# Kernel tuning notes

Measured on AMD Instinct MI355X. Metric: run time of the kernel, lower is better.

The kernel has to match this reference:

```python
import jax, jax.numpy as jnp
import numpy as np

EMBEDDING_LOSS_WEIGHT = 1.0
COMMITMENT_LOSS_WEIGHT = 0.25
ENTROPY_LOSS_WEIGHT = 0.02


def setup_inputs() -> dict:
    key = jax.random.key(0)
    k1, k2 = jax.random.split(key)
    inputs = jax.random.normal(k1, (16, 32, 32, 256), dtype=jnp.float32)
    # RandomUniform() default range in keras is [-0.05, 0.05]
    codebook = jax.random.uniform(k2, (4096, 256), dtype=jnp.float32,
                                  minval=-0.05, maxval=0.05)
    return {"inputs": inputs, "codebook": codebook}


def reference(inputs, codebook):
    sg = jax.lax.stop_gradient
    B, H, W, D = inputs.shape
    K = codebook.shape[0]
    flat = inputs.reshape(-1, D)  # [N, D], N = B*H*W

    x_sq = jnp.sum(flat * flat, axis=-1, keepdims=True)          # [N, 1]
    c_sq = jnp.sum(codebook * codebook, axis=-1)                 # [K]
    cross = flat @ codebook.T                                    # [N, K] GEMM
    distances = x_sq + c_sq - 2.0 * cross                        # [N, K]

    tokens = jnp.argmin(distances, axis=-1)                      # [N] int32
    embeddings = jnp.take(codebook, tokens, axis=0).reshape(B, H, W, D)

    embedding_loss = EMBEDDING_LOSS_WEIGHT * jnp.mean((sg(embeddings) - inputs) ** 2)
    commitment_loss = COMMITMENT_LOSS_WEIGHT * jnp.mean((embeddings - sg(inputs)) ** 2)

    # entropy loss: for codebook entries never selected, penalize their
    # minimum distance to any input vector
    active = jnp.zeros((K,), jnp.int32).at[tokens].add(1)        # scatter counts
    min_dist_per_class = jnp.min(distances, axis=0)              # [K]
    entropy_loss = ENTROPY_LOSS_WEIGHT * jnp.mean(
        jnp.where(active == 0, min_dist_per_class, 0.0))

    loss = embedding_loss + commitment_loss + entropy_loss

    # training=True straight-through estimator
    out = inputs + sg(embeddings - inputs)
    return out, loss
```

## Files before the change

### kernel.cpp

```cpp
#include <hip/hip_runtime.h>
#include <stdint.h>


#define N_ROWS 16384
#define DIM    256
#define KCODES 4096
#define NCHUNK 8
#define KC     (KCODES / NCHUNK)
#define TM     128
#define TN     128
#define BK     32
#define NKT    (KC / TN)
#define NDC    (DIM / BK)
#define NSTEP  (NKT * NDC)
#define NGRAN  (NCHUNK * 2)
#define NRB    (N_ROWS / TM)

typedef float    f32x4 __attribute__((ext_vector_type(4)));
typedef _Float16 f16x8 __attribute__((ext_vector_type(8)));

#define GLOAD_LDS16(g, l) __builtin_amdgcn_global_load_lds(                 \
    (const __attribute__((address_space(1))) void*)(g),                     \
    (__attribute__((address_space(3))) void*)(l), 16, 0, 0)

#define WAITVM_(n) asm volatile("s_waitcnt vmcnt(" #n ")" ::: "memory")
#define WAITVM(n)  WAITVM_(n)
#define MEMPIN()   asm volatile("" ::: "memory")

__device__ __forceinline__ unsigned umin_(unsigned a, unsigned b) { return a < b ? a : b; }
__device__ __forceinline__ unsigned umax_(unsigned a, unsigned b) { return a > b ? a : b; }
__device__ __forceinline__ unsigned long long umin64_(unsigned long long a,
                                                      unsigned long long b) {
    return a < b ? a : b;
}
__device__ __forceinline__ unsigned long long umax64_(unsigned long long a,
                                                      unsigned long long b) {
    return a > b ? a : b;
}

__device__ __forceinline__ unsigned fkey(float f) {
    unsigned b = __float_as_uint(f);
    return (b & 0x80000000u) ? ~b : (b | 0x80000000u);
}
__device__ __forceinline__ float fkey_inv(unsigned k) {
    unsigned b = (k & 0x80000000u) ? (k ^ 0x80000000u) : ~k;
    return __uint_as_float(b);
}
__device__ __forceinline__ unsigned short f2h(float f) {
    union { _Float16 h; unsigned short u; } cv;
    cv.h = (_Float16)f;
    return cv.u;
}

__global__ __launch_bounds__(256) void vq_prep_kernel(
        const float* __restrict__ x, const float* __restrict__ cb,
        unsigned short* __restrict__ xh, unsigned short* __restrict__ ch,
        float* __restrict__ xsq, float* __restrict__ csq,
        unsigned* __restrict__ active, double* __restrict__ accum,
        unsigned* __restrict__ counter) {
    const int b = blockIdx.x, t = threadIdx.x;
    if (b < KCODES / 256) {
        int i = b * 256 + t;
        active[i] = 0u;
        if (i == 0) { accum[0] = 0.0; accum[1] = 0.0; counter[0] = 0u; }
    }
    const size_t NX = (size_t)N_ROWS * DIM;
    size_t e = (size_t)b * 1024 + (size_t)t * 4;
    const float* src; unsigned short* dst; float* sq; size_t off;
    if (e < NX) { src = x;  dst = xh; sq = xsq; off = e; }
    else        { src = cb; dst = ch; sq = csq; off = e - NX; }
    float4 v = *(const float4*)(src + off);
    ushort4 h;
    h.x = f2h(v.x); h.y = f2h(v.y); h.z = f2h(v.z); h.w = f2h(v.w);
    *(ushort4*)(dst + off) = h;
    double s = (double)v.x * v.x + (double)v.y * v.y
             + (double)v.z * v.z + (double)v.w * v.w;
    for (int o = 32; o; o >>= 1) s += __shfl_down(s, o);
    if ((t & 63) == 0) sq[off >> 8] = (float)s;
}

__global__ __launch_bounds__(256, 2) void vq_gemm_kernel(
        const unsigned short* __restrict__ xh_g, const unsigned short* __restrict__ ch_g,
        const float* __restrict__ xsq, const float* __restrict__ csq,
        unsigned* __restrict__ colmin_part, uint2* __restrict__ top2_out) {
    __shared__ __align__(16) unsigned short b_lds[4][TN][BK];
    __shared__ float    xsq_l[128];
    __shared__ float    csq_l[KC];
    __shared__ unsigned colmin_l[KC];
    __shared__ uint2    u12_l[16][256];

    const int t = threadIdx.x;
    const int wave = t >> 6, lane = t & 63, quad = lane >> 4, L = lane & 15;
    const int whalf = wave >> 1, chalf = wave & 1;
    const int row0  = blockIdx.x * TM;
    const int code0 = blockIdx.y * KC;

    if (t < 128) xsq_l[t] = xsq[row0 + t];
    csq_l[t]       = csq[code0 + t];
    csq_l[t + 256] = csq[code0 + t + 256];
    colmin_l[t] = 0xFFFFFFFFu; colmin_l[t + 256] = 0xFFFFFFFFu;
#pragma unroll
    for (int i = 0; i < 16; ++i)
        u12_l[i][t] = make_uint2(0xFFFFFFFFu, 0xFFFFFFFFu);

    const unsigned short* abase =
        xh_g + ((size_t)(row0 + whalf * 64 + L) * DIM + quad * 8);

    auto stageB = [&](int buf, int kt_, int dc_) {
        const unsigned short* bsrc =
            ch_g + (size_t)(code0 + kt_ * TN) * DIM + dc_ * BK;
        unsigned short* dst = &b_lds[buf][0][0];
#pragma unroll
        for (int k = 0; k < 2; ++k) {
            const int j = t + k * 256;
            const int r = j >> 2, sg = (j & 3) ^ ((j >> 3) & 3);
            GLOAD_LDS16(bsrc + (size_t)r * DIM + sg * 8, dst + (size_t)j * 8);
        }
    };

    const int bslot = (L >> 1) & 3;

    f16x8 afr[NDC][4];
#pragma unroll
    for (int dc = 0; dc < NDC; ++dc)
#pragma unroll
        for (int mt = 0; mt < 4; ++mt)
            afr[dc][mt] = *(const f16x8*)(abase + (size_t)mt * 16 * DIM + dc * BK);
    MEMPIN();
    stageB(0, 0, 0);
    MEMPIN();
    stageB(1, 0, 1);
    MEMPIN();
    stageB(2, 0, 2);
    MEMPIN();

    asm volatile("s_waitcnt lgkmcnt(0)" ::: "memory");
    __builtin_amdgcn_s_barrier();
    __builtin_amdgcn_sched_barrier(0);

    auto epilogue = [&](int kt, f32x4 (&acc)[4][4]) {
        float csq4[4]; unsigned colf[4];
        float dmin[4] = {3.4e38f, 3.4e38f, 3.4e38f, 3.4e38f};
#pragma unroll
        for (int nt = 0; nt < 4; ++nt) {
            csq4[nt] = csq_l[kt * TN + chalf * 64 + nt * 16 + L];
            colf[nt] = (unsigned)(kt * 128 + chalf * 64 + nt * 16 + L);
        }
#pragma unroll
        for (int mt = 0; mt < 4; ++mt) {
            const f32x4 xq = *(const f32x4*)&xsq_l[whalf * 64 + mt * 16 + quad * 4];
#pragma unroll
            for (int reg = 0; reg < 4; ++reg) {
                const int i = mt * 4 + reg;
                uint2 e = u12_l[i][t];
#pragma unroll
                for (int nt = 0; nt < 4; ++nt) {
                    float s = fmaf(-2.0f, acc[mt][nt][reg], csq4[nt]);
                    unsigned key = (fkey(s) & 0xFFFFFE00u) | colf[nt];
                    unsigned lo = umin_(e.x, key);
                    e.y = umin_(e.y, umax_(e.x, key));
                    e.x = lo;
                    dmin[nt] = fminf(dmin[nt], xq[reg] + s);
                }
                u12_l[i][t] = e;
            }
        }
#pragma unroll
        for (int nt = 0; nt < 4; ++nt) {
            unsigned dk = fkey(dmin[nt]);
            dk = umin_(dk, (unsigned)__shfl_xor((int)dk, 16));
            dk = umin_(dk, (unsigned)__shfl_xor((int)dk, 32));
            if (quad == 0)
                atomicMin(&colmin_l[kt * TN + chalf * 64 + nt * 16 + L], dk);
        }
    };

    for (int kt = 0; kt < NKT; ++kt) {
        f32x4 acc[4][4];
#pragma unroll
        for (int mt = 0; mt < 4; ++mt)
#pragma unroll
            for (int nt = 0; nt < 4; ++nt) acc[mt][nt] = (f32x4){0.f, 0.f, 0.f, 0.f};
#pragma unroll
        for (int dc = 0; dc < NDC; ++dc) {
            WAITVM(4);
            __builtin_amdgcn_s_barrier();
            __builtin_amdgcn_sched_barrier(0);
            stageB((dc + 3) & 3, (kt + (dc >= 5)) & 3, (dc + 3) & 7);
            f16x8 bf[4];
#pragma unroll
            for (int nt = 0; nt < 4; ++nt)
                bf[nt] = *(const f16x8*)
                    &b_lds[dc & 3][chalf * 64 + nt * 16 + L][(quad ^ bslot) * 8];
#pragma unroll
            for (int mt = 0; mt < 4; ++mt)
#pragma unroll
                for (int nt = 0; nt < 4; ++nt)
                    acc[mt][nt] = __builtin_amdgcn_mfma_f32_16x16x32_f16(
                        afr[dc][mt], bf[nt], acc[mt][nt], 0, 0, 0);
        }
        epilogue(kt, acc);
    }

    unsigned u1[16], u2[16];
#pragma unroll
    for (int i = 0; i < 16; ++i) {
        uint2 e = u12_l[i][t];
        u1[i] = e.x; u2[i] = e.y;
    }
#pragma unroll
    for (int i = 0; i < 16; ++i) {
#pragma unroll
        for (int st = 1; st < 16; st <<= 1) {
            unsigned w1 = (unsigned)__shfl_xor((int)u1[i], st);
            unsigned w2 = (unsigned)__shfl_xor((int)u2[i], st);
            unsigned a = umin_(u1[i], w1), b = umax_(u1[i], w1);
            u1[i] = a;
            u2[i] = umin_(umin_(u2[i], w2), b);
        }
    }
    if (L == 0) {
        const size_t gbase = (size_t)(blockIdx.y * 2 + chalf) * N_ROWS;
#pragma unroll
        for (int mt = 0; mt < 4; ++mt)
#pragma unroll
            for (int reg = 0; reg < 4; ++reg) {
                const int row = row0 + whalf * 64 + mt * 16 + quad * 4 + reg;
                top2_out[gbase + row] = make_uint2(u1[mt * 4 + reg], u2[mt * 4 + reg]);
            }
    }

    __syncthreads();
    unsigned* cp = colmin_part + (size_t)blockIdx.x * KCODES + code0;
    cp[t]       = colmin_l[t];
    cp[t + 256] = colmin_l[t + 256];
}

__global__ __launch_bounds__(256) void vq_refine_kernel(
        const float* __restrict__ x, const float* __restrict__ cb,
        const uint2* __restrict__ top2, unsigned* __restrict__ active,
        float* __restrict__ out, double* __restrict__ accum) {
    __shared__ double wsum[4];
    const int wave = threadIdx.x >> 6, lane = threadIdx.x & 63;
    const int row  = blockIdx.x * 4 + wave;

    const int g = (lane >> 1) & 15;
    uint2 e = top2[(size_t)g * N_ROWS + row];
    unsigned key = (lane & 1) ? e.y : e.x;
    unsigned idc = (unsigned)((g >> 1) * KC) + (key & 0x1FFu);
    unsigned long long pk =
        ((unsigned long long)(key & 0xFFFFFE00u) << 32) | idc;
    if (lane >= 32) pk = ~0ull;

    unsigned long long m1 = pk, m2 = ~0ull;
#pragma unroll
    for (int o = 1; o < 64; o <<= 1) {
        unsigned long long w1 = (unsigned long long)__shfl_xor((long long)m1, o);
        unsigned long long w2 = (unsigned long long)__shfl_xor((long long)m2, o);
        unsigned long long lo = umin64_(m1, w1), hi = umax64_(m1, w1);
        m1 = lo;
        m2 = umin64_(umin64_(m2, w2), hi);
    }
    const float v0 = fkey_inv((unsigned)(m1 >> 32));
    const float v1 = fkey_inv((unsigned)(m2 >> 32));

    float4 xv = ((const float4*)(x + (size_t)row * DIM))[lane];
    int tok;
    if (v1 > v0 + 1.0e-2f) {
        tok = (int)(unsigned)(m1 & 0xFFFFFFFFu);
    } else {
        int id8[8];
        unsigned long long cur = pk;
#pragma unroll
        for (int k = 0; k < 8; ++k) {
            unsigned long long m = cur;
#pragma unroll
            for (int o = 1; o < 64; o <<= 1)
                m = umin64_(m, (unsigned long long)__shfl_xor((long long)m, o));
            id8[k] = (int)(unsigned)(m & 0xFFFFFFFFu);
            if (cur == m) cur = ~0ull;
        }

        double xs64 = (double)xv.x * xv.x + (double)xv.y * xv.y
                    + (double)xv.z * xv.z + (double)xv.w * xv.w;
        double p[8];
#pragma unroll
        for (int k = 0; k < 8; ++k) {
            float4 c4 = ((const float4*)(cb + (size_t)id8[k] * DIM))[lane];
            double dd  = (double)xv.x * c4.x + (double)xv.y * c4.y
                       + (double)xv.z * c4.z + (double)xv.w * c4.w;
            double cc2 = (double)c4.x * c4.x + (double)c4.y * c4.y
                       + (double)c4.z * c4.z + (double)c4.w * c4.w;
            p[k] = cc2 - 2.0 * dd;
        }
#pragma unroll
        for (int o = 32; o; o >>= 1) {
            xs64 += __shfl_down(xs64, o);
#pragma unroll
            for (int k = 0; k < 8; ++k)
                p[k] += __shfl_down(p[k], o);
        }
        if (lane == 0) {
            double D[8], Dmin = 1e300;
#pragma unroll
            for (int k = 0; k < 8; ++k) {
                D[k] = xs64 + p[k];
                Dmin = fmin(Dmin, D[k]);
            }
            int e2; frexp(Dmin, &e2);
            double U   = ldexp(1.0, e2 - 1 - 23);
            double thr = Dmin + 0.75 * U;
            tok = 0x7FFFFFFF;
#pragma unroll
            for (int k = 0; k < 8; ++k)
                if (D[k] <= thr && id8[k] < tok) tok = id8[k];
        }
        tok = __shfl(tok, 0);
    }

    if (lane == 0) active[tok] = 1u;
    float4 sel = ((const float4*)(cb + (size_t)tok * DIM))[lane];
    ((float4*)out)[(size_t)row * 64 + lane] = sel;
    float dx = sel.x - xv.x, dy = sel.y - xv.y, dz = sel.z - xv.z, dw = sel.w - xv.w;
    float s = dx * dx + dy * dy + dz * dz + dw * dw;
    for (int o = 32; o; o >>= 1) s += __shfl_down(s, o);
    if (lane == 0) wsum[wave] = (double)s;
    __syncthreads();
    if (threadIdx.x == 0) atomicAdd(accum, wsum[0] + wsum[1] + wsum[2] + wsum[3]);
}

__global__ __launch_bounds__(256) void vq_final_kernel(
        const unsigned* __restrict__ colmin_part, const unsigned* __restrict__ active,
        double* __restrict__ accum, unsigned* __restrict__ counter,
        float* __restrict__ out) {
    __shared__ double red[256];
    const int t = threadIdx.x;
    const int c = blockIdx.x * 256 + t;
    unsigned m = 0xFFFFFFFFu;
#pragma unroll 8
    for (int rb = 0; rb < NRB; ++rb)
        m = umin_(m, colmin_part[(size_t)rb * KCODES + c]);
    red[t] = (active[c] == 0u) ? (double)fkey_inv(m) : 0.0;
    __syncthreads();
    for (int o = 128; o; o >>= 1) {
        if (t < o) red[t] += red[t + o];
        __syncthreads();
    }
    if (t == 0) {
        atomicAdd(&accum[1], red[0]);
        __threadfence();
        unsigned old = atomicAdd(counter, 1u);
        if (old == 15u) {
            __threadfence();
            double ent = atomicAdd(&accum[1], 0.0);
            double loss = 1.25 * (accum[0] / (double)((size_t)N_ROWS * DIM))
                        + 0.02 * (ent / (double)KCODES);
            out[(size_t)N_ROWS * DIM] = (float)loss;
        }
    }
}

extern "C" void kernel_launch(void* const* d_in, const int* in_sizes, int n_in,
                              void* d_out, int out_size, void* d_ws, size_t ws_size,
                              hipStream_t stream) {
    const float* x  = (const float*)d_in[0];
    const float* cb = (const float*)d_in[1];
    float* out = (float*)d_out;

    char* ws = (char*)d_ws;
    float*    xsq     = (float*)(ws + 0);
    float*    csq     = (float*)(ws + 65536);
    unsigned* active  = (unsigned*)(ws + 81920);
    double*   accum   = (double*)(ws + 98304);
    unsigned* counter = (unsigned*)(ws + 98560);
    uint2*    top2    = (uint2*)(ws + 131072);
    unsigned* cpart   = (unsigned*)(ws + 2228224);
    unsigned short* xh_g = (unsigned short*)(ws + 4325376);
    unsigned short* ch_g = (unsigned short*)(ws + 12713984);

    vq_prep_kernel<<<((N_ROWS + KCODES) * DIM) / 1024, 256, 0, stream>>>(
        x, cb, xh_g, ch_g, xsq, csq, active, accum, counter);
    vq_gemm_kernel<<<dim3(NRB, NCHUNK), 256, 0, stream>>>(
        xh_g, ch_g, xsq, csq, cpart, top2);
    vq_refine_kernel<<<N_ROWS / 4, 256, 0, stream>>>(
        x, cb, top2, active, out, accum);
    vq_final_kernel<<<KCODES / 256, 256, 0, stream>>>(
        cpart, active, accum, counter, out);
}
```

Baseline: 204.0 us.

## Halve A-fragment registers and B buffering to fit three GEMM blocks per CU

The GEMM kernel stops holding all eight A fragments in registers and instead loads A in two halves per code tile. B staging drops from a 4-deep to a 2-deep LDS ring with simple __syncthreads double buffering. Launch bounds go from 2 to 3 blocks per CU so more blocks can be resident. A is now reloaded from global for every code tile instead of once, and the hand-tuned vmcnt pipelining is gone. The final kernel is also split across more blocks, with 64 columns per block and a 4-way partial min, to spread the column-min reduction.

Result: slower. 248.9 us (+22.0%).

```diff
diff --git a/kernel.cpp b/kernel.cpp
--- a/kernel.cpp
+++ b/kernel.cpp
@@ -23,10 +23,6 @@
     (const __attribute__((address_space(1))) void*)(g),                     \
     (__attribute__((address_space(3))) void*)(l), 16, 0, 0)
 
-#define WAITVM_(n) asm volatile("s_waitcnt vmcnt(" #n ")" ::: "memory")
-#define WAITVM(n)  WAITVM_(n)
-#define MEMPIN()   asm volatile("" ::: "memory")
-
 __device__ __forceinline__ unsigned umin_(unsigned a, unsigned b) { return a < b ? a : b; }
 __device__ __forceinline__ unsigned umax_(unsigned a, unsigned b) { return a > b ? a : b; }
 __device__ __forceinline__ unsigned long long umin64_(unsigned long long a,
@@ -79,11 +75,11 @@
     if ((t & 63) == 0) sq[off >> 8] = (float)s;
 }
 
-__global__ __launch_bounds__(256, 2) void vq_gemm_kernel(
+__global__ __launch_bounds__(256, 3) void vq_gemm_kernel(
         const unsigned short* __restrict__ xh_g, const unsigned short* __restrict__ ch_g,
         const float* __restrict__ xsq, const float* __restrict__ csq,
         unsigned* __restrict__ colmin_part, uint2* __restrict__ top2_out) {
-    __shared__ __align__(16) unsigned short b_lds[4][TN][BK];
+    __shared__ __align__(16) unsigned short b_lds[2][TN][BK];
     __shared__ float    xsq_l[128];
     __shared__ float    csq_l[KC];
     __shared__ unsigned colmin_l[KC];
@@ -120,23 +116,17 @@
 
     const int bslot = (L >> 1) & 3;
 
-    f16x8 afr[NDC][4];
-#pragma unroll
-    for (int dc = 0; dc < NDC; ++dc)
-#pragma unroll
-        for (int mt = 0; mt < 4; ++mt)
-            afr[dc][mt] = *(const f16x8*)(abase + (size_t)mt * 16 * DIM + dc * BK);
-    MEMPIN();
+    f16x8 afr[4][4];
+    auto loadA = [&](int h) {
+#pragma unroll
+        for (int i = 0; i < 4; ++i)
+#pragma unroll
+            for (int mt = 0; mt < 4; ++mt)
+                afr[i][mt] = *(const f16x8*)(abase + (size_t)mt * 16 * DIM
+                                             + (h * 4 + i) * BK);
+    };
+
     stageB(0, 0, 0);
-    MEMPIN();
-    stageB(1, 0, 1);
-    MEMPIN();
-    stageB(2, 0, 2);
-    MEMPIN();
-
-    asm volatile("s_waitcnt lgkmcnt(0)" ::: "memory");
-    __builtin_amdgcn_s_barrier();
-    __builtin_amdgcn_sched_barrier(0);
 
     auto epilogue = [&](int kt, f32x4 (&acc)[4][4]) {
         float csq4[4]; unsigned colf[4];
@@ -181,23 +171,46 @@
         for (int mt = 0; mt < 4; ++mt)
 #pragma unroll
             for (int nt = 0; nt < 4; ++nt) acc[mt][nt] = (f32x4){0.f, 0.f, 0.f, 0.f};
-#pragma unroll
-        for (int dc = 0; dc < NDC; ++dc) {
-            WAITVM(4);
-            __builtin_amdgcn_s_barrier();
-            __builtin_amdgcn_sched_barrier(0);
-            stageB((dc + 3) & 3, (kt + (dc >= 5)) & 3, (dc + 3) & 7);
+
+        loadA(0);
+#pragma unroll
+        for (int dc = 0; dc < 4; ++dc) {
+            const int cur = dc & 1;
+            __syncthreads();
+            const int s = kt * NDC + dc;
+            if (s < NSTEP - 1)
+                stageB(cur ^ 1, kt + (dc == NDC - 1), (dc + 1) & 7);
             f16x8 bf[4];
 #pragma unroll
             for (int nt = 0; nt < 4; ++nt)
                 bf[nt] = *(const f16x8*)
-                    &b_lds[dc & 3][chalf * 64 + nt * 16 + L][(quad ^ bslot) * 8];
+                    &b_lds[cur][chalf * 64 + nt * 16 + L][(quad ^ bslot) * 8];
 #pragma unroll
             for (int mt = 0; mt < 4; ++mt)
 #pragma unroll
                 for (int nt = 0; nt < 4; ++nt)
                     acc[mt][nt] = __builtin_amdgcn_mfma_f32_16x16x32_f16(
                         afr[dc][mt], bf[nt], acc[mt][nt], 0, 0, 0);
+        }
+        loadA(1);
+#pragma unroll
+        for (int dc = 4; dc < 8; ++dc) {
+            const int cur = dc & 1;
+            __syncthreads();
+            const int s = kt * NDC + dc;
+            if (s < NSTEP - 1)
+                stageB(cur ^ 1, kt + (dc == NDC - 1), (dc + 1) & 7);
+            f16x8 bf[4];
+#pragma unroll
+            for (int nt = 0; nt < 4; ++nt)
+                bf[nt] = *(const f16x8*)
+                    &b_lds[cur][chalf * 64 + nt * 16 + L][(quad ^ bslot) * 8];
+#pragma unroll
+            for (int mt = 0; mt < 4; ++mt)
+#pragma unroll
+                for (int nt = 0; nt < 4; ++nt)
+                    acc[mt][nt] = __builtin_amdgcn_mfma_f32_16x16x32_f16(
+                        afr[dc - 4][mt], bf[nt], acc[mt][nt], 0, 0, 0);
         }
         epilogue(kt, acc);
     }
@@ -333,29 +346,37 @@
         const unsigned* __restrict__ colmin_part, const unsigned* __restrict__ active,
         double* __restrict__ accum, unsigned* __restrict__ counter,
         float* __restrict__ out) {
-    __shared__ double red[256];
+    __shared__ unsigned pmin[4][64];
+    __shared__ double red[64];
     const int t = threadIdx.x;
-    const int c = blockIdx.x * 256 + t;
+    const int cl = t & 63, part = t >> 6;
+    const int c = blockIdx.x * 64 + cl;
     unsigned m = 0xFFFFFFFFu;
 #pragma unroll 8
-    for (int rb = 0; rb < NRB; ++rb)
+    for (int rb = part * 32; rb < part * 32 + 32; ++rb)
         m = umin_(m, colmin_part[(size_t)rb * KCODES + c]);
-    red[t] = (active[c] == 0u) ? (double)fkey_inv(m) : 0.0;
+    pmin[part][cl] = m;
     __syncthreads();
-    for (int o = 128; o; o >>= 1) {
-        if (t < o) red[t] += red[t + o];
-        __syncthreads();
-    }
-    if (t == 0) {
-        atomicAdd(&accum[1], red[0]);
-        __threadfence();
-        unsigned old = atomicAdd(counter, 1u);
-        if (old == 15u) {
+    if (part == 0) {
+        m = umin_(umin_(pmin[0][cl], pmin[1][cl]),
+                  umin_(pmin[2][cl], pmin[3][cl]));
+        red[cl] = (active[c] == 0u) ? (double)fkey_inv(m) : 0.0;
+    }
+    __syncthreads();
+    if (t < 64) {
+        double s = red[t];
+        for (int o = 32; o; o >>= 1) s += __shfl_down(s, o);
+        if (t == 0) {
+            atomicAdd(&accum[1], s);
             __threadfence();
-            double ent = atomicAdd(&accum[1], 0.0);
-            double loss = 1.25 * (accum[0] / (double)((size_t)N_ROWS * DIM))
-                        + 0.02 * (ent / (double)KCODES);
-            out[(size_t)N_ROWS * DIM] = (float)loss;
+            unsigned old = atomicAdd(counter, 1u);
+            if (old == 63u) {
+                __threadfence();
+                double ent = atomicAdd(&accum[1], 0.0);
+                double loss = 1.25 * (accum[0] / (double)((size_t)N_ROWS * DIM))
+                            + 0.02 * (ent / (double)KCODES);
+                out[(size_t)N_ROWS * DIM] = (float)loss;
+            }
         }
     }
 }
@@ -384,6 +405,6 @@
         xh_g, ch_g, xsq, csq, cpart, top2);
     vq_refine_kernel<<<N_ROWS / 4, 256, 0, stream>>>(
         x, cb, top2, active, out, accum);
-    vq_final_kernel<<<KCODES / 256, 256, 0, stream>>>(
+    vq_final_kernel<<<KCODES / 64, 256, 0, stream>>>(
         cpart, active, accum, counter, out);
 }
```
